# Kernel optimization log

Measured on AMD Instinct MI355X. Metric: run time of the kernel, lower is better.

The kernel has to match this reference:

```python
import jax, jax.numpy as jnp
import numpy as np

PARAM = 10.0
EPS = 1e-06

def _feature_map(t):
    # elus_feature_map: param*relu(x) + (exp(param*min(x,0)) - 1) + 1
    x1 = jax.nn.relu(t)
    x2 = t - x1  # negative part
    return PARAM * x1 + jnp.exp(PARAM * x2)

def setup_inputs() -> dict:
    key = jax.random.key(0)
    ks = jax.random.split(key, 7)
    B, C, H, W = 8, 512, 128, 128
    d = C // 8
    s = 1.0 / np.sqrt(C)
    return {
        "x":  jax.random.normal(ks[0], (B, C, H, W), dtype=jnp.float32),
        "Wq": jax.random.normal(ks[1], (d, C), dtype=jnp.float32) * s,
        "bq": jax.random.normal(ks[2], (d,), dtype=jnp.float32) * 0.01,
        "Wk": jax.random.normal(ks[3], (d, C), dtype=jnp.float32) * s,
        "bk": jax.random.normal(ks[4], (d,), dtype=jnp.float32) * 0.01,
        "Wv": jax.random.normal(ks[5], (C, C), dtype=jnp.float32) * s,
        "bv": jax.random.normal(ks[6], (C,), dtype=jnp.float32) * 0.01,
        "gamma": jnp.full((1,), 0.5, dtype=jnp.float32),
    }

def reference(x, Wq, bq, Wk, bk, Wv, bv, gamma):
    B, C, H, W = x.shape
    N = H * W
    xf = x.reshape(B, C, N)  # flatten spatial; 1x1 convs become matmuls
    Q = jnp.einsum('dc,bcn->bdn', Wq, xf) + bq[None, :, None]   # [B, d, N]
    K = jnp.einsum('dc,bcn->bdn', Wk, xf) + bk[None, :, None]   # [B, d, N]
    V = jnp.einsum('oc,bcn->bon', Wv, xf) + bv[None, :, None]   # [B, C, N]
    Q = jnp.transpose(_feature_map(Q), (0, 2, 1))               # [B, N, d]
    K = _feature_map(K)                                         # [B, d, N]
    KV = jnp.einsum('bmn,bcn->bmc', K, V)                       # [B, d, C]
    norm = 1.0 / jnp.einsum('bnc,bc->bn', Q, jnp.sum(K, axis=-1) + EPS)  # [B, N]
    wv = jnp.einsum('bnm,bmc,bn->bcn', Q, KV, norm)             # [B, C, N]
    wv = wv.reshape(B, C, H, W)
    return x + gamma * wv
```

## Files before the change

### kernel.cpp

```cpp
#include <hip/hip_runtime.h>
#include <hip/hip_bf16.h>
#include <cstdint>

typedef __bf16 bf16x8 __attribute__((ext_vector_type(8)));
typedef float f32x4 __attribute__((ext_vector_type(4)));

#define DEV static __device__ __forceinline__

constexpr int NB = 8;
constexpr int NC = 512;
constexpr int NS = 16384;
constexpr int ND = 64;
constexpr int SK = 32;
constexpr float FPARAM = 10.0f;
constexpr float FEPS = 1e-6f;

DEV unsigned short f2bf(float f) {
  uint32_t u = __builtin_bit_cast(uint32_t, f);
  u += 0x7fffu + ((u >> 16) & 1u);
  return (unsigned short)(u >> 16);
}
DEV float bf2f(unsigned short h) {
  uint32_t u = ((uint32_t)h) << 16;
  return __builtin_bit_cast(float, u);
}
DEV float fmap(float t) {
  float p = fmaxf(t, 0.0f);
  float m = fminf(t, 0.0f);
  return FPARAM * p + __expf(FPARAM * m);
}

DEV void tile_store4(unsigned short* t, int row, int k, ushort4 v) {
  int ch = (k >> 3) ^ (row & 7);
  *(ushort4*)(t + row * 64 + ch * 8 + (k & 7)) = v;
}
DEV void tile_store8(unsigned short* t, int row, int k, uint4 v) {
  int ch = (k >> 3) ^ (row & 7);
  *(uint4*)(t + row * 64 + ch * 8) = v;
}
DEV bf16x8 tile_frag(const unsigned short* t, int row, int k) {
  int ch = (k >> 3) ^ (row & 7);
  uint4 u = *(const uint4*)(t + row * 64 + ch * 8);
  return __builtin_bit_cast(bf16x8, u);
}
DEV f32x4 mfma16(bf16x8 a, bf16x8 b, f32x4 c) {
  return __builtin_amdgcn_mfma_f32_16x16x32_bf16(a, b, c, 0, 0, 0);
}

__global__ __launch_bounds__(256) void kernelA(
    const float* __restrict__ x, const float* __restrict__ Wq,
    const float* __restrict__ bq, const float* __restrict__ Wk,
    const float* __restrict__ bk, unsigned short* __restrict__ Kp,
    unsigned short* __restrict__ Qt) {
  __shared__ unsigned short sW[128 * 64];
  __shared__ unsigned short sX[128 * 64];
  const int t = threadIdx.x;
  const int lane = t & 63, wave = t >> 6;
  const int wm = wave >> 1, wn = wave & 1;
  const int l15 = lane & 15, q = lane >> 4;
  const int n0 = blockIdx.x * 128;
  const int b = blockIdx.y;
  const float* xb = x + (size_t)b * NC * NS;

  f32x4 acc[4][4];
  const f32x4 zero = {0.f, 0.f, 0.f, 0.f};
  for (int i = 0; i < 4; i++)
    for (int j = 0; j < 4; j++) acc[i][j] = zero;

  const int qq = t & 3, grp = t >> 2;
  const int n4 = (grp & 31) * 4, cb = (grp >> 5) * 4;
  const int shfl_base = (t & 63) & ~3;

  for (int c0 = 0; c0 < NC; c0 += 64) {
    __syncthreads();
    {
      int f4 = t & 15;
      for (int it = 0; it < 8; it++) {
        int row = (t >> 4) + it * 16;
        const float* src = (row < 64) ? (Wq + (size_t)row * NC + c0 + f4 * 4)
                                      : (Wk + (size_t)(row - 64) * NC + c0 + f4 * 4);
        float4 v = *(const float4*)src;
        tile_store4(sW, row, f4 * 4,
                    make_ushort4(f2bf(v.x), f2bf(v.y), f2bf(v.z), f2bf(v.w)));
      }
    }
    for (int it = 0; it < 8; it++) {
      int c_l = cb + qq + it * 8;
      float4 v = *(const float4*)(xb + (size_t)(c0 + c_l) * NS + n0 + n4);
      float vv[4] = {v.x, v.y, v.z, v.w};
      float o[4];
      for (int r = 0; r < 4; r++) {
        int j = (qq + r) & 3;
        float send = vv[(qq - r) & 3];
        o[j] = __shfl(send, shfl_base + j);
      }
      tile_store4(sX, n4 + qq, it * 8 + cb,
                  make_ushort4(f2bf(o[0]), f2bf(o[1]), f2bf(o[2]), f2bf(o[3])));
    }
    __syncthreads();
    for (int kk = 0; kk < 64; kk += 32) {
      int kb = kk + q * 8;
      bf16x8 af[4], bg[4];
      for (int i = 0; i < 4; i++) af[i] = tile_frag(sW, wm * 64 + i * 16 + l15, kb);
      for (int j = 0; j < 4; j++) bg[j] = tile_frag(sX, wn * 64 + j * 16 + l15, kb);
      for (int i = 0; i < 4; i++)
        for (int j = 0; j < 4; j++) acc[i][j] = mfma16(af[i], bg[j], acc[i][j]);
    }
  }

  if (wm == 0) {
    for (int i = 0; i < 4; i++) {
      int mb = i * 16 + q * 4;
      float b0 = bq[mb + 0], b1 = bq[mb + 1], b2 = bq[mb + 2], b3 = bq[mb + 3];
      for (int j = 0; j < 4; j++) {
        int n = n0 + wn * 64 + j * 16 + l15;
        f32x4 v = acc[i][j];
        ushort4 o = make_ushort4(f2bf(fmap(v[0] + b0)), f2bf(fmap(v[1] + b1)),
                                 f2bf(fmap(v[2] + b2)), f2bf(fmap(v[3] + b3)));
        *(ushort4*)(Qt + ((size_t)b * NS + n) * ND + mb) = o;
      }
    }
  } else {
    for (int i = 0; i < 4; i++) {
      int mb = i * 16 + q * 4;
      float b0 = bk[mb + 0], b1 = bk[mb + 1], b2 = bk[mb + 2], b3 = bk[mb + 3];
      for (int j = 0; j < 4; j++) {
        int n = n0 + wn * 64 + j * 16 + l15;
        f32x4 v = acc[i][j];
        Kp[((size_t)b * ND + mb + 0) * NS + n] = f2bf(fmap(v[0] + b0));
        Kp[((size_t)b * ND + mb + 1) * NS + n] = f2bf(fmap(v[1] + b1));
        Kp[((size_t)b * ND + mb + 2) * NS + n] = f2bf(fmap(v[2] + b2));
        Kp[((size_t)b * ND + mb + 3) * NS + n] = f2bf(fmap(v[3] + b3));
      }
    }
  }
}

__global__ __launch_bounds__(256) void kernelB(
    const float* __restrict__ x, const unsigned short* __restrict__ Kp,
    float* __restrict__ Pp, float* __restrict__ KsP) {
  __shared__ unsigned short sK[64 * 64];
  __shared__ unsigned short sX[256 * 64];
  __shared__ float sSum[64];
  const int t = threadIdx.x;
  const int lane = t & 63, wave = t >> 6;
  const int l15 = lane & 15, q = lane >> 4;
  const int s = blockIdx.x, half = blockIdx.y, b = blockIdx.z;
  const int cp0 = half * 256;
  const int nbase = s * (NS / SK);
  if (t < 64) sSum[t] = 0.0f;

  f32x4 acc[4][4];
  const f32x4 zero = {0.f, 0.f, 0.f, 0.f};
  for (int i = 0; i < 4; i++)
    for (int j = 0; j < 4; j++) acc[i][j] = zero;

  for (int nc = 0; nc < NS / SK; nc += 64) {
    int n0 = nbase + nc;
    __syncthreads();
    for (int it = 0; it < 2; it++) {
      int row = (t >> 3) + it * 32;
      int ch = t & 7;
      uint4 v = *(const uint4*)(Kp + ((size_t)b * ND + row) * NS + n0 + ch * 8);
      tile_store8(sK, row, ch * 8, v);
      if (half == 0) {
        const unsigned short* pv = (const unsigned short*)&v;
        float ssum = 0.f;
        for (int e = 0; e < 8; e++) ssum += bf2f(pv[e]);
        atomicAdd(&sSum[row], ssum);
      }
    }
    {
      int f4 = t & 15;
      for (int it = 0; it < 16; it++) {
        int row = (t >> 4) + it * 16;
        float4 v = *(const float4*)(x + ((size_t)b * NC + cp0 + row) * NS + n0 + f4 * 4);
        tile_store4(sX, row, f4 * 4,
                    make_ushort4(f2bf(v.x), f2bf(v.y), f2bf(v.z), f2bf(v.w)));
      }
    }
    __syncthreads();
    for (int kk = 0; kk < 64; kk += 32) {
      int kb = kk + q * 8;
      bf16x8 af[4], bg[4];
      for (int i = 0; i < 4; i++) af[i] = tile_frag(sK, i * 16 + l15, kb);
      for (int j = 0; j < 4; j++) bg[j] = tile_frag(sX, wave * 64 + j * 16 + l15, kb);
      for (int i = 0; i < 4; i++)
        for (int j = 0; j < 4; j++) acc[i][j] = mfma16(af[i], bg[j], acc[i][j]);
    }
  }
  for (int i = 0; i < 4; i++) {
    int mb = i * 16 + q * 4;
    for (int j = 0; j < 4; j++) {
      int cp = cp0 + wave * 64 + j * 16 + l15;
      f32x4 v = acc[i][j];
      for (int r = 0; r < 4; r++)
        Pp[(((size_t)b * SK + s) * ND + mb + r) * NC + cp] = v[r];
    }
  }
  __syncthreads();
  if (half == 0 && t < 64) KsP[((size_t)b * SK + s) * ND + t] = sSum[t];
}

__global__ __launch_bounds__(256) void kernelC1(
    const float* __restrict__ Pp, const float* __restrict__ KsP,
    float* __restrict__ KXt, float* __restrict__ Ksum) {
  const int m = blockIdx.x, b = blockIdx.y, t = threadIdx.x;
  float a0 = 0.f, a1 = 0.f;
  for (int s = 0; s < SK; s++) {
    const float* p = Pp + (((size_t)b * SK + s) * ND + m) * NC;
    a0 += p[t];
    a1 += p[t + 256];
  }
  float* o = KXt + ((size_t)b * ND + m) * NC;
  o[t] = a0;
  o[t + 256] = a1;
  if (t == 0) {
    float ks = 0.f;
    for (int s = 0; s < SK; s++) ks += KsP[((size_t)b * SK + s) * ND + m];
    Ksum[b * ND + m] = ks;
  }
}

__global__ __launch_bounds__(64) void kernelC2(
    const float* __restrict__ KXt, const float* __restrict__ Wv,
    const float* __restrict__ bv, const float* __restrict__ Ksum,
    unsigned short* __restrict__ KVT) {
  __shared__ unsigned short sA[64 * 64];
  __shared__ unsigned short sB[64 * 64];
  const int t = threadIdx.x;
  const int l15 = t & 15, q = t >> 4;
  const int ct = blockIdx.x, b = blockIdx.y;
  f32x4 acc[4][4];
  const f32x4 zero = {0.f, 0.f, 0.f, 0.f};
  for (int i = 0; i < 4; i++)
    for (int j = 0; j < 4; j++) acc[i][j] = zero;

  for (int c0 = 0; c0 < NC; c0 += 64) {
    __syncthreads();
    int f4 = t & 15;
    for (int it = 0; it < 16; it++) {
      int row = (t >> 4) + it * 4;
      float4 v = *(const float4*)(Wv + ((size_t)(ct * 64 + row)) * NC + c0 + f4 * 4);
      tile_store4(sA, row, f4 * 4,
                  make_ushort4(f2bf(v.x), f2bf(v.y), f2bf(v.z), f2bf(v.w)));
      float4 w = *(const float4*)(KXt + ((size_t)b * ND + row) * NC + c0 + f4 * 4);
      tile_store4(sB, row, f4 * 4,
                  make_ushort4(f2bf(w.x), f2bf(w.y), f2bf(w.z), f2bf(w.w)));
    }
    __syncthreads();
    for (int kk = 0; kk < 64; kk += 32) {
      int kb = kk + q * 8;
      bf16x8 af[4], bg[4];
      for (int i = 0; i < 4; i++) af[i] = tile_frag(sA, i * 16 + l15, kb);
      for (int j = 0; j < 4; j++) bg[j] = tile_frag(sB, j * 16 + l15, kb);
      for (int i = 0; i < 4; i++)
        for (int j = 0; j < 4; j++) acc[i][j] = mfma16(af[i], bg[j], acc[i][j]);
    }
  }
  for (int j = 0; j < 4; j++) {
    int m = j * 16 + l15;
    float ks = Ksum[b * ND + m];
    for (int i = 0; i < 4; i++) {
      for (int r = 0; r < 4; r++) {
        int c = ct * 64 + i * 16 + q * 4 + r;
        float v = acc[i][j][r] + ks * bv[c];
        KVT[((size_t)b * NC + c) * ND + m] = f2bf(v);
      }
    }
  }
}

__global__ __launch_bounds__(256) void kernelD(
    const float* __restrict__ x, const unsigned short* __restrict__ Qt,
    const unsigned short* __restrict__ KVT, const float* __restrict__ Ksum,
    const float* __restrict__ gamma, float* __restrict__ out) {
  __shared__ unsigned short sA[256 * 64];
  __shared__ unsigned short sB[128 * 64];
  __shared__ float sN[128];
  __shared__ float sKs[64];
  const int t = threadIdx.x;
  const int lane = t & 63, wave = t >> 6;
  const int wm = wave >> 1, wn = wave & 1;
  const int l15 = lane & 15, q = lane >> 4;
  const int n0 = blockIdx.x * 128;
  const int c0 = blockIdx.y * 256;
  const int b = blockIdx.z;
  if (t < 64) sKs[t] = Ksum[b * ND + t] + FEPS;
  {
    int ch = t & 7;
    for (int it = 0; it < 8; it++) {
      int row = (t >> 3) + it * 32;
      uint4 v = *(const uint4*)(KVT + ((size_t)b * NC + c0 + row) * ND + ch * 8);
      tile_store8(sA, row, ch * 8, v);
    }
    for (int it = 0; it < 4; it++) {
      int row = (t >> 3) + it * 32;
      uint4 v = *(const uint4*)(Qt + ((size_t)b * NS + n0 + row) * ND + ch * 8);
      tile_store8(sB, row, ch * 8, v);
    }
  }
  __syncthreads();
  if (t < 128) {
    float sum = 0.f;
    for (int ch = 0; ch < 8; ch++) {
      const unsigned short* p = sB + t * 64 + ((ch ^ (t & 7)) * 8);
      for (int e = 0; e < 8; e++) sum += bf2f(p[e]) * sKs[ch * 8 + e];
    }
    sN[t] = 1.0f / sum;
  }
  __syncthreads();

  f32x4 acc[8][4];
  const f32x4 zero = {0.f, 0.f, 0.f, 0.f};
  for (int i = 0; i < 8; i++)
    for (int j = 0; j < 4; j++) acc[i][j] = zero;
  for (int kk = 0; kk < 64; kk += 32) {
    int kb = kk + q * 8;
    bf16x8 af[8], bg[4];
    for (int i = 0; i < 8; i++) af[i] = tile_frag(sA, wm * 128 + i * 16 + l15, kb);
    for (int j = 0; j < 4; j++) bg[j] = tile_frag(sB, wn * 64 + j * 16 + l15, kb);
    for (int i = 0; i < 8; i++)
      for (int j = 0; j < 4; j++) acc[i][j] = mfma16(af[i], bg[j], acc[i][j]);
  }
  float g = gamma[0];
  for (int i = 0; i < 8; i++) {
    int cb = c0 + wm * 128 + i * 16 + q * 4;
    for (int j = 0; j < 4; j++) {
      int nl = wn * 64 + j * 16 + l15;
      int n = n0 + nl;
      float nr = sN[nl] * g;
      f32x4 v = acc[i][j];
      for (int r = 0; r < 4; r++) {
        size_t idx = ((size_t)b * NC + cb + r) * NS + n;
        out[idx] = x[idx] + nr * v[r];
      }
    }
  }
}

extern "C" void kernel_launch(void* const* d_in, const int* in_sizes, int n_in,
                              void* d_out, int out_size, void* d_ws, size_t ws_size,
                              hipStream_t stream) {
  (void)in_sizes; (void)n_in; (void)out_size; (void)ws_size;
  const float* x = (const float*)d_in[0];
  const float* Wq = (const float*)d_in[1];
  const float* bq = (const float*)d_in[2];
  const float* Wk = (const float*)d_in[3];
  const float* bk = (const float*)d_in[4];
  const float* Wv = (const float*)d_in[5];
  const float* bv = (const float*)d_in[6];
  const float* gamma = (const float*)d_in[7];
  float* out = (float*)d_out;

  char* ws = (char*)d_ws;
  unsigned short* Qt = (unsigned short*)ws;  ws += (size_t)NB * NS * ND * 2;
  unsigned short* Kp = (unsigned short*)ws;  ws += (size_t)NB * ND * NS * 2;
  float* Pp = (float*)ws;                    ws += (size_t)NB * SK * ND * NC * 4;
  float* KsP = (float*)ws;                   ws += (size_t)NB * SK * ND * 4;
  float* KXt = (float*)ws;                   ws += (size_t)NB * ND * NC * 4;
  float* Ksum = (float*)ws;                  ws += (size_t)NB * ND * 4;
  unsigned short* KVT = (unsigned short*)ws; ws += (size_t)NB * NC * ND * 2;

  kernelA<<<dim3(NS / 128, NB), dim3(256), 0, stream>>>(x, Wq, bq, Wk, bk, Kp, Qt);
  kernelB<<<dim3(SK, 2, NB), dim3(256), 0, stream>>>(x, Kp, Pp, KsP);
  kernelC1<<<dim3(ND, NB), dim3(256), 0, stream>>>(Pp, KsP, KXt, Ksum);
  kernelC2<<<dim3(NC / 64, NB), dim3(64), 0, stream>>>(KXt, Wv, bv, Ksum, KVT);
  kernelD<<<dim3(NS / 128, NC / 256, NB), dim3(256), 0, stream>>>(x, Qt, KVT, Ksum, gamma, out);
}
```

Before: 640.6 us.

## Pre-convert weights to bf16, drop LDS staging, fuse K-sum into projection kernel

Adds a prep kernel that converts Wq/Wk/Wv to bf16 once per call, so the projection and KV kernels read bf16 weight fragments straight from global memory. The K column-sum moves into kernelA's epilogue through wave shuffles and global atomics, which removes the partial-sum buffer and its reduction. kernelB, C2 and D drop shared-memory tiles and load MFMA fragments directly from global memory. kernelA double-buffers x in registers and LDS, and block indices are remapped for locality. The cost is an extra launch, float atomics whose summation order is nondeterministic, and uncoalesced direct global fragment loads.

After: 683.1 us. 6.6% more time.

```diff
diff --git a/kernel.cpp b/kernel.cpp
--- a/kernel.cpp
+++ b/kernel.cpp
@@ -1,9 +1,9 @@
 #include <hip/hip_runtime.h>
-#include <hip/hip_bf16.h>
 #include <cstdint>
 
 typedef __bf16 bf16x8 __attribute__((ext_vector_type(8)));
 typedef float f32x4 __attribute__((ext_vector_type(4)));
+typedef unsigned short u16x8 __attribute__((ext_vector_type(8)));
 
 #define DEV static __device__ __forceinline__
 
@@ -29,31 +29,58 @@
   float m = fminf(t, 0.0f);
   return FPARAM * p + __expf(FPARAM * m);
 }
+DEV f32x4 mfma16(bf16x8 a, bf16x8 b, f32x4 c) {
+  return __builtin_amdgcn_mfma_f32_16x16x32_bf16(a, b, c, 0, 0, 0);
+}
+DEV bf16x8 ld_bf8(const unsigned short* p) {
+  uint4 u = *(const uint4*)p;
+  return __builtin_bit_cast(bf16x8, u);
+}
+DEV bf16x8 cvt8(float4 a, float4 b) {
+  u16x8 t;
+  t[0] = f2bf(a.x); t[1] = f2bf(a.y); t[2] = f2bf(a.z); t[3] = f2bf(a.w);
+  t[4] = f2bf(b.x); t[5] = f2bf(b.y); t[6] = f2bf(b.z); t[7] = f2bf(b.w);
+  return __builtin_bit_cast(bf16x8, t);
+}
 
 DEV void tile_store4(unsigned short* t, int row, int k, ushort4 v) {
   int ch = (k >> 3) ^ (row & 7);
   *(ushort4*)(t + row * 64 + ch * 8 + (k & 7)) = v;
-}
-DEV void tile_store8(unsigned short* t, int row, int k, uint4 v) {
-  int ch = (k >> 3) ^ (row & 7);
-  *(uint4*)(t + row * 64 + ch * 8) = v;
 }
 DEV bf16x8 tile_frag(const unsigned short* t, int row, int k) {
   int ch = (k >> 3) ^ (row & 7);
   uint4 u = *(const uint4*)(t + row * 64 + ch * 8);
   return __builtin_bit_cast(bf16x8, u);
 }
-DEV f32x4 mfma16(bf16x8 a, bf16x8 b, f32x4 c) {
-  return __builtin_amdgcn_mfma_f32_16x16x32_bf16(a, b, c, 0, 0, 0);
+
+__global__ __launch_bounds__(256) void kernelP(
+    const float* __restrict__ Wq, const float* __restrict__ Wk,
+    const float* __restrict__ Wv, unsigned short* __restrict__ Wqkb,
+    unsigned short* __restrict__ Wvb, float* __restrict__ Ksum) {
+  const int tid = blockIdx.x * 256 + threadIdx.x;
+  const int stride = gridDim.x * 256;
+  if (tid < NB * ND) Ksum[tid] = 0.f;
+  for (int p = tid; p < ND * NC / 4; p += stride) {
+    float4 v = ((const float4*)Wq)[p];
+    ((ushort4*)Wqkb)[p] = make_ushort4(f2bf(v.x), f2bf(v.y), f2bf(v.z), f2bf(v.w));
+  }
+  for (int p = tid; p < ND * NC / 4; p += stride) {
+    float4 v = ((const float4*)Wk)[p];
+    ((ushort4*)(Wqkb + ND * NC))[p] =
+        make_ushort4(f2bf(v.x), f2bf(v.y), f2bf(v.z), f2bf(v.w));
+  }
+  for (int p = tid; p < NC * NC / 4; p += stride) {
+    float4 v = ((const float4*)Wv)[p];
+    ((ushort4*)Wvb)[p] = make_ushort4(f2bf(v.x), f2bf(v.y), f2bf(v.z), f2bf(v.w));
+  }
 }
 
 __global__ __launch_bounds__(256) void kernelA(
-    const float* __restrict__ x, const float* __restrict__ Wq,
-    const float* __restrict__ bq, const float* __restrict__ Wk,
-    const float* __restrict__ bk, unsigned short* __restrict__ Kp,
-    unsigned short* __restrict__ Qt) {
-  __shared__ unsigned short sW[128 * 64];
-  __shared__ unsigned short sX[128 * 64];
+    const float* __restrict__ x, const unsigned short* __restrict__ Wqk,
+    const float* __restrict__ bq, const float* __restrict__ bk,
+    unsigned short* __restrict__ Kp, unsigned short* __restrict__ Qt,
+    float* __restrict__ Ksum) {
+  __shared__ unsigned short sX[2][128 * 64];
   const int t = threadIdx.x;
   const int lane = t & 63, wave = t >> 6;
   const int wm = wave >> 1, wn = wave & 1;
@@ -69,49 +96,59 @@
 
   const int qq = t & 3, grp = t >> 2;
   const int n4 = (grp & 31) * 4, cb = (grp >> 5) * 4;
-  const int shfl_base = (t & 63) & ~3;
-
-  for (int c0 = 0; c0 < NC; c0 += 64) {
-    __syncthreads();
-    {
-      int f4 = t & 15;
-      for (int it = 0; it < 8; it++) {
-        int row = (t >> 4) + it * 16;
-        const float* src = (row < 64) ? (Wq + (size_t)row * NC + c0 + f4 * 4)
-                                      : (Wk + (size_t)(row - 64) * NC + c0 + f4 * 4);
-        float4 v = *(const float4*)src;
-        tile_store4(sW, row, f4 * 4,
-                    make_ushort4(f2bf(v.x), f2bf(v.y), f2bf(v.z), f2bf(v.w)));
-      }
-    }
+  const int shfl_base = lane & ~3;
+
+  float4 pf[8];
+#pragma unroll
+  for (int it = 0; it < 8; it++)
+    pf[it] = *(const float4*)(xb + (size_t)(cb + qq + it * 8) * NS + n0 + n4);
+
+  for (int cc = 0; cc < 8; cc++) {
+    unsigned short* sx = sX[cc & 1];
+    const int c0 = cc * 64;
+#pragma unroll
     for (int it = 0; it < 8; it++) {
-      int c_l = cb + qq + it * 8;
-      float4 v = *(const float4*)(xb + (size_t)(c0 + c_l) * NS + n0 + n4);
+      float4 v = pf[it];
       float vv[4] = {v.x, v.y, v.z, v.w};
       float o[4];
+#pragma unroll
       for (int r = 0; r < 4; r++) {
         int j = (qq + r) & 3;
         float send = vv[(qq - r) & 3];
         o[j] = __shfl(send, shfl_base + j);
       }
-      tile_store4(sX, n4 + qq, it * 8 + cb,
+      tile_store4(sx, n4 + qq, it * 8 + cb,
                   make_ushort4(f2bf(o[0]), f2bf(o[1]), f2bf(o[2]), f2bf(o[3])));
     }
+    if (cc < 7) {
+      const int c1 = c0 + 64;
+#pragma unroll
+      for (int it = 0; it < 8; it++)
+        pf[it] = *(const float4*)(xb + (size_t)(c1 + cb + qq + it * 8) * NS + n0 + n4);
+    }
     __syncthreads();
+#pragma unroll
     for (int kk = 0; kk < 64; kk += 32) {
       int kb = kk + q * 8;
       bf16x8 af[4], bg[4];
-      for (int i = 0; i < 4; i++) af[i] = tile_frag(sW, wm * 64 + i * 16 + l15, kb);
-      for (int j = 0; j < 4; j++) bg[j] = tile_frag(sX, wn * 64 + j * 16 + l15, kb);
+#pragma unroll
       for (int i = 0; i < 4; i++)
+        af[i] = ld_bf8(Wqk + (size_t)(wm * 64 + i * 16 + l15) * NC + c0 + kb);
+#pragma unroll
+      for (int j = 0; j < 4; j++) bg[j] = tile_frag(sx, wn * 64 + j * 16 + l15, kb);
+#pragma unroll
+      for (int i = 0; i < 4; i++)
+#pragma unroll
         for (int j = 0; j < 4; j++) acc[i][j] = mfma16(af[i], bg[j], acc[i][j]);
     }
   }
 
   if (wm == 0) {
+#pragma unroll
     for (int i = 0; i < 4; i++) {
       int mb = i * 16 + q * 4;
       float b0 = bq[mb + 0], b1 = bq[mb + 1], b2 = bq[mb + 2], b3 = bq[mb + 3];
+#pragma unroll
       for (int j = 0; j < 4; j++) {
         int n = n0 + wn * 64 + j * 16 + l15;
         f32x4 v = acc[i][j];
@@ -121,16 +158,35 @@
       }
     }
   } else {
+#pragma unroll
     for (int i = 0; i < 4; i++) {
       int mb = i * 16 + q * 4;
       float b0 = bk[mb + 0], b1 = bk[mb + 1], b2 = bk[mb + 2], b3 = bk[mb + 3];
+      float ks0 = 0.f, ks1 = 0.f, ks2 = 0.f, ks3 = 0.f;
+#pragma unroll
       for (int j = 0; j < 4; j++) {
         int n = n0 + wn * 64 + j * 16 + l15;
         f32x4 v = acc[i][j];
-        Kp[((size_t)b * ND + mb + 0) * NS + n] = f2bf(fmap(v[0] + b0));
-        Kp[((size_t)b * ND + mb + 1) * NS + n] = f2bf(fmap(v[1] + b1));
-        Kp[((size_t)b * ND + mb + 2) * NS + n] = f2bf(fmap(v[2] + b2));
-        Kp[((size_t)b * ND + mb + 3) * NS + n] = f2bf(fmap(v[3] + b3));
+        float f0 = fmap(v[0] + b0), f1 = fmap(v[1] + b1);
+        float f2 = fmap(v[2] + b2), f3 = fmap(v[3] + b3);
+        Kp[((size_t)b * ND + mb + 0) * NS + n] = f2bf(f0);
+        Kp[((size_t)b * ND + mb + 1) * NS + n] = f2bf(f1);
+        Kp[((size_t)b * ND + mb + 2) * NS + n] = f2bf(f2);
+        Kp[((size_t)b * ND + mb + 3) * NS + n] = f2bf(f3);
+        ks0 += f0; ks1 += f1; ks2 += f2; ks3 += f3;
+      }
+#pragma unroll
+      for (int ms = 1; ms < 16; ms <<= 1) {
+        ks0 += __shfl_xor(ks0, ms);
+        ks1 += __shfl_xor(ks1, ms);
+        ks2 += __shfl_xor(ks2, ms);
+        ks3 += __shfl_xor(ks3, ms);
+      }
+      if (l15 == 0) {
+        atomicAdd(&Ksum[b * ND + mb + 0], ks0);
+        atomicAdd(&Ksum[b * ND + mb + 1], ks1);
+        atomicAdd(&Ksum[b * ND + mb + 2], ks2);
+        atomicAdd(&Ksum[b * ND + mb + 3], ks3);
       }
     }
   }
@@ -138,75 +194,59 @@
 
 __global__ __launch_bounds__(256) void kernelB(
     const float* __restrict__ x, const unsigned short* __restrict__ Kp,
-    float* __restrict__ Pp, float* __restrict__ KsP) {
-  __shared__ unsigned short sK[64 * 64];
-  __shared__ unsigned short sX[256 * 64];
-  __shared__ float sSum[64];
+    float* __restrict__ Pp) {
   const int t = threadIdx.x;
   const int lane = t & 63, wave = t >> 6;
   const int l15 = lane & 15, q = lane >> 4;
-  const int s = blockIdx.x, half = blockIdx.y, b = blockIdx.z;
-  const int cp0 = half * 256;
+  const int id = blockIdx.x, b = blockIdx.y;
+  const int s = ((id >> 5) << 3) + (id & 7);
+  const int quarter = (id >> 3) & 3;
   const int nbase = s * (NS / SK);
-  if (t < 64) sSum[t] = 0.0f;
-
-  f32x4 acc[4][4];
+  const unsigned short* kpb = Kp + (size_t)b * ND * NS;
+  const float* xq = x + ((size_t)b * NC + quarter * 128 + wave * 32) * NS;
+
+  f32x4 acc[4][2];
   const f32x4 zero = {0.f, 0.f, 0.f, 0.f};
   for (int i = 0; i < 4; i++)
-    for (int j = 0; j < 4; j++) acc[i][j] = zero;
-
-  for (int nc = 0; nc < NS / SK; nc += 64) {
-    int n0 = nbase + nc;
-    __syncthreads();
-    for (int it = 0; it < 2; it++) {
-      int row = (t >> 3) + it * 32;
-      int ch = t & 7;
-      uint4 v = *(const uint4*)(Kp + ((size_t)b * ND + row) * NS + n0 + ch * 8);
-      tile_store8(sK, row, ch * 8, v);
-      if (half == 0) {
-        const unsigned short* pv = (const unsigned short*)&v;
-        float ssum = 0.f;
-        for (int e = 0; e < 8; e++) ssum += bf2f(pv[e]);
-        atomicAdd(&sSum[row], ssum);
-      }
-    }
-    {
-      int f4 = t & 15;
-      for (int it = 0; it < 16; it++) {
-        int row = (t >> 4) + it * 16;
-        float4 v = *(const float4*)(x + ((size_t)b * NC + cp0 + row) * NS + n0 + f4 * 4);
-        tile_store4(sX, row, f4 * 4,
-                    make_ushort4(f2bf(v.x), f2bf(v.y), f2bf(v.z), f2bf(v.w)));
-      }
-    }
-    __syncthreads();
-    for (int kk = 0; kk < 64; kk += 32) {
-      int kb = kk + q * 8;
-      bf16x8 af[4], bg[4];
-      for (int i = 0; i < 4; i++) af[i] = tile_frag(sK, i * 16 + l15, kb);
-      for (int j = 0; j < 4; j++) bg[j] = tile_frag(sX, wave * 64 + j * 16 + l15, kb);
-      for (int i = 0; i < 4; i++)
-        for (int j = 0; j < 4; j++) acc[i][j] = mfma16(af[i], bg[j], acc[i][j]);
-    }
-  }
+    for (int j = 0; j < 2; j++) acc[i][j] = zero;
+
+#pragma unroll 2
+  for (int nc = 0; nc < NS / SK; nc += 32) {
+    int nb = nbase + nc + q * 8;
+    bf16x8 af[4], bg[2];
+#pragma unroll
+    for (int i = 0; i < 4; i++)
+      af[i] = ld_bf8(kpb + (size_t)(i * 16 + l15) * NS + nb);
+#pragma unroll
+    for (int j = 0; j < 2; j++) {
+      const float* px = xq + (size_t)(j * 16 + l15) * NS + nb;
+      bg[j] = cvt8(*(const float4*)px, *(const float4*)(px + 4));
+    }
+#pragma unroll
+    for (int i = 0; i < 4; i++)
+#pragma unroll
+      for (int j = 0; j < 2; j++) acc[i][j] = mfma16(af[i], bg[j], acc[i][j]);
+  }
+
+  float* pp = Pp + ((size_t)b * SK + s) * ND * NC;
+#pragma unroll
   for (int i = 0; i < 4; i++) {
     int mb = i * 16 + q * 4;
-    for (int j = 0; j < 4; j++) {
-      int cp = cp0 + wave * 64 + j * 16 + l15;
+#pragma unroll
+    for (int j = 0; j < 2; j++) {
+      int cp = quarter * 128 + wave * 32 + j * 16 + l15;
       f32x4 v = acc[i][j];
-      for (int r = 0; r < 4; r++)
-        Pp[(((size_t)b * SK + s) * ND + mb + r) * NC + cp] = v[r];
-    }
-  }
-  __syncthreads();
-  if (half == 0 && t < 64) KsP[((size_t)b * SK + s) * ND + t] = sSum[t];
+#pragma unroll
+      for (int r = 0; r < 4; r++) pp[(size_t)(mb + r) * NC + cp] = v[r];
+    }
+  }
 }
 
 __global__ __launch_bounds__(256) void kernelC1(
-    const float* __restrict__ Pp, const float* __restrict__ KsP,
-    float* __restrict__ KXt, float* __restrict__ Ksum) {
+    const float* __restrict__ Pp, float* __restrict__ KXt) {
   const int m = blockIdx.x, b = blockIdx.y, t = threadIdx.x;
   float a0 = 0.f, a1 = 0.f;
+#pragma unroll 8
   for (int s = 0; s < SK; s++) {
     const float* p = Pp + (((size_t)b * SK + s) * ND + m) * NC;
     a0 += p[t];
@@ -215,57 +255,52 @@
   float* o = KXt + ((size_t)b * ND + m) * NC;
   o[t] = a0;
   o[t + 256] = a1;
-  if (t == 0) {
-    float ks = 0.f;
-    for (int s = 0; s < SK; s++) ks += KsP[((size_t)b * SK + s) * ND + m];
-    Ksum[b * ND + m] = ks;
-  }
-}
-
-__global__ __launch_bounds__(64) void kernelC2(
-    const float* __restrict__ KXt, const float* __restrict__ Wv,
+}
+
+__global__ __launch_bounds__(256) void kernelC2(
+    const float* __restrict__ KXt, const unsigned short* __restrict__ Wvb,
     const float* __restrict__ bv, const float* __restrict__ Ksum,
     unsigned short* __restrict__ KVT) {
-  __shared__ unsigned short sA[64 * 64];
-  __shared__ unsigned short sB[64 * 64];
   const int t = threadIdx.x;
-  const int l15 = t & 15, q = t >> 4;
+  const int lane = t & 63, wave = t >> 6;
+  const int wm = wave >> 1, wn = wave & 1;
+  const int l15 = lane & 15, q = lane >> 4;
   const int ct = blockIdx.x, b = blockIdx.y;
-  f32x4 acc[4][4];
+
+  f32x4 acc[2][2];
   const f32x4 zero = {0.f, 0.f, 0.f, 0.f};
-  for (int i = 0; i < 4; i++)
-    for (int j = 0; j < 4; j++) acc[i][j] = zero;
-
-  for (int c0 = 0; c0 < NC; c0 += 64) {
-    __syncthreads();
-    int f4 = t & 15;
-    for (int it = 0; it < 16; it++) {
-      int row = (t >> 4) + it * 4;
-      float4 v = *(const float4*)(Wv + ((size_t)(ct * 64 + row)) * NC + c0 + f4 * 4);
-      tile_store4(sA, row, f4 * 4,
-                  make_ushort4(f2bf(v.x), f2bf(v.y), f2bf(v.z), f2bf(v.w)));
-      float4 w = *(const float4*)(KXt + ((size_t)b * ND + row) * NC + c0 + f4 * 4);
-      tile_store4(sB, row, f4 * 4,
-                  make_ushort4(f2bf(w.x), f2bf(w.y), f2bf(w.z), f2bf(w.w)));
-    }
-    __syncthreads();
-    for (int kk = 0; kk < 64; kk += 32) {
-      int kb = kk + q * 8;
-      bf16x8 af[4], bg[4];
-      for (int i = 0; i < 4; i++) af[i] = tile_frag(sA, i * 16 + l15, kb);
-      for (int j = 0; j < 4; j++) bg[j] = tile_frag(sB, j * 16 + l15, kb);
-      for (int i = 0; i < 4; i++)
-        for (int j = 0; j < 4; j++) acc[i][j] = mfma16(af[i], bg[j], acc[i][j]);
-    }
-  }
-  for (int j = 0; j < 4; j++) {
-    int m = j * 16 + l15;
-    float ks = Ksum[b * ND + m];
-    for (int i = 0; i < 4; i++) {
+  for (int i = 0; i < 2; i++)
+    for (int j = 0; j < 2; j++) acc[i][j] = zero;
+
+#pragma unroll 2
+  for (int c0 = 0; c0 < NC; c0 += 32) {
+    int kb = c0 + q * 8;
+    bf16x8 af[2], bg[2];
+#pragma unroll
+    for (int i = 0; i < 2; i++)
+      af[i] = ld_bf8(Wvb + (size_t)(ct * 64 + wm * 32 + i * 16 + l15) * NC + kb);
+#pragma unroll
+    for (int j = 0; j < 2; j++) {
+      const float* px = KXt + ((size_t)b * ND + wn * 32 + j * 16 + l15) * NC + kb;
+      bg[j] = cvt8(*(const float4*)px, *(const float4*)(px + 4));
+    }
+#pragma unroll
+    for (int i = 0; i < 2; i++)
+#pragma unroll
+      for (int j = 0; j < 2; j++) acc[i][j] = mfma16(af[i], bg[j], acc[i][j]);
+  }
+
+#pragma unroll
+  for (int j = 0; j < 2; j++) {
+    int m = wn * 32 + j * 16 + l15;
+    float km = Ksum[b * ND + m];
+#pragma unroll
+    for (int i = 0; i < 2; i++) {
+      f32x4 v = acc[i][j];
+#pragma unroll
       for (int r = 0; r < 4; r++) {
-        int c = ct * 64 + i * 16 + q * 4 + r;
-        float v = acc[i][j][r] + ks * bv[c];
-        KVT[((size_t)b * NC + c) * ND + m] = f2bf(v);
+        int c = ct * 64 + wm * 32 + i * 16 + q * 4 + r;
+        KVT[((size_t)b * NC + c) * ND + m] = f2bf(v[r] + km * bv[c]);
       }
     }
   }
@@ -275,65 +310,70 @@
     const float* __restrict__ x, const unsigned short* __restrict__ Qt,
     const unsigned short* __restrict__ KVT, const float* __restrict__ Ksum,
     const float* __restrict__ gamma, float* __restrict__ out) {
-  __shared__ unsigned short sA[256 * 64];
-  __shared__ unsigned short sB[128 * 64];
   __shared__ float sN[128];
   __shared__ float sKs[64];
   const int t = threadIdx.x;
   const int lane = t & 63, wave = t >> 6;
   const int wm = wave >> 1, wn = wave & 1;
   const int l15 = lane & 15, q = lane >> 4;
-  const int n0 = blockIdx.x * 128;
-  const int c0 = blockIdx.y * 256;
-  const int b = blockIdx.z;
+  const int id = blockIdx.x, b = blockIdx.y;
+  const int nblk = ((id >> 4) << 3) + (id & 7);
+  const int chalf = (id >> 3) & 1;
+  const int n0 = nblk * 128, c0 = chalf * 256;
+
   if (t < 64) sKs[t] = Ksum[b * ND + t] + FEPS;
-  {
-    int ch = t & 7;
-    for (int it = 0; it < 8; it++) {
-      int row = (t >> 3) + it * 32;
-      uint4 v = *(const uint4*)(KVT + ((size_t)b * NC + c0 + row) * ND + ch * 8);
-      tile_store8(sA, row, ch * 8, v);
-    }
-    for (int it = 0; it < 4; it++) {
-      int row = (t >> 3) + it * 32;
-      uint4 v = *(const uint4*)(Qt + ((size_t)b * NS + n0 + row) * ND + ch * 8);
-      tile_store8(sB, row, ch * 8, v);
-    }
-  }
   __syncthreads();
   if (t < 128) {
+    const unsigned short* qrow = Qt + ((size_t)b * NS + n0 + t) * ND;
     float sum = 0.f;
-    for (int ch = 0; ch < 8; ch++) {
-      const unsigned short* p = sB + t * 64 + ((ch ^ (t & 7)) * 8);
-      for (int e = 0; e < 8; e++) sum += bf2f(p[e]) * sKs[ch * 8 + e];
+#pragma unroll
+    for (int mm = 0; mm < 64; mm += 8) {
+      uint4 u = *(const uint4*)(qrow + mm);
+      const unsigned short* us = (const unsigned short*)&u;
+#pragma unroll
+      for (int e = 0; e < 8; e++) sum += bf2f(us[e]) * sKs[mm + e];
     }
     sN[t] = 1.0f / sum;
   }
   __syncthreads();
 
-  f32x4 acc[8][4];
-  const f32x4 zero = {0.f, 0.f, 0.f, 0.f};
-  for (int i = 0; i < 8; i++)
-    for (int j = 0; j < 4; j++) acc[i][j] = zero;
-  for (int kk = 0; kk < 64; kk += 32) {
-    int kb = kk + q * 8;
-    bf16x8 af[8], bg[4];
-    for (int i = 0; i < 8; i++) af[i] = tile_frag(sA, wm * 128 + i * 16 + l15, kb);
-    for (int j = 0; j < 4; j++) bg[j] = tile_frag(sB, wn * 64 + j * 16 + l15, kb);
-    for (int i = 0; i < 8; i++)
-      for (int j = 0; j < 4; j++) acc[i][j] = mfma16(af[i], bg[j], acc[i][j]);
-  }
-  float g = gamma[0];
-  for (int i = 0; i < 8; i++) {
-    int cb = c0 + wm * 128 + i * 16 + q * 4;
-    for (int j = 0; j < 4; j++) {
-      int nl = wn * 64 + j * 16 + l15;
-      int n = n0 + nl;
-      float nr = sN[nl] * g;
-      f32x4 v = acc[i][j];
-      for (int r = 0; r < 4; r++) {
-        size_t idx = ((size_t)b * NC + cb + r) * NS + n;
-        out[idx] = x[idx] + nr * v[r];
+  const float g = gamma[0];
+#pragma unroll 1
+  for (int h = 0; h < 2; h++) {
+    f32x4 acc[4][4];
+    const f32x4 zero = {0.f, 0.f, 0.f, 0.f};
+    for (int i = 0; i < 4; i++)
+      for (int j = 0; j < 4; j++) acc[i][j] = zero;
+#pragma unroll
+    for (int kk = 0; kk < 64; kk += 32) {
+      int kb = kk + q * 8;
+      bf16x8 af[4], bg[4];
+#pragma unroll
+      for (int i = 0; i < 4; i++)
+        af[i] = ld_bf8(KVT +
+                       ((size_t)b * NC + c0 + wm * 128 + h * 64 + i * 16 + l15) * ND + kb);
+#pragma unroll
+      for (int j = 0; j < 4; j++)
+        bg[j] = ld_bf8(Qt + ((size_t)b * NS + n0 + wn * 64 + j * 16 + l15) * ND + kb);
+#pragma unroll
+      for (int i = 0; i < 4; i++)
+#pragma unroll
+        for (int j = 0; j < 4; j++) acc[i][j] = mfma16(af[i], bg[j], acc[i][j]);
+    }
+#pragma unroll
+    for (int i = 0; i < 4; i++) {
+      int cb = c0 + wm * 128 + h * 64 + i * 16 + q * 4;
+#pragma unroll
+      for (int j = 0; j < 4; j++) {
+        int nl = wn * 64 + j * 16 + l15;
+        float nr = sN[nl] * g;
+        size_t base = ((size_t)b * NC + cb) * NS + n0 + nl;
+        f32x4 v = acc[i][j];
+#pragma unroll
+        for (int r = 0; r < 4; r++) {
+          size_t idx = base + (size_t)r * NS;
+          out[idx] = x[idx] + nr * v[r];
+        }
       }
     }
   }
@@ -357,14 +397,16 @@
   unsigned short* Qt = (unsigned short*)ws;  ws += (size_t)NB * NS * ND * 2;
   unsigned short* Kp = (unsigned short*)ws;  ws += (size_t)NB * ND * NS * 2;
   float* Pp = (float*)ws;                    ws += (size_t)NB * SK * ND * NC * 4;
-  float* KsP = (float*)ws;                   ws += (size_t)NB * SK * ND * 4;
   float* KXt = (float*)ws;                   ws += (size_t)NB * ND * NC * 4;
   float* Ksum = (float*)ws;                  ws += (size_t)NB * ND * 4;
   unsigned short* KVT = (unsigned short*)ws; ws += (size_t)NB * NC * ND * 2;
-
-  kernelA<<<dim3(NS / 128, NB), dim3(256), 0, stream>>>(x, Wq, bq, Wk, bk, Kp, Qt);
-  kernelB<<<dim3(SK, 2, NB), dim3(256), 0, stream>>>(x, Kp, Pp, KsP);
-  kernelC1<<<dim3(ND, NB), dim3(256), 0, stream>>>(Pp, KsP, KXt, Ksum);
-  kernelC2<<<dim3(NC / 64, NB), dim3(64), 0, stream>>>(KXt, Wv, bv, Ksum, KVT);
-  kernelD<<<dim3(NS / 128, NC / 256, NB), dim3(256), 0, stream>>>(x, Qt, KVT, Ksum, gamma, out);
-}
+  unsigned short* Wqkb = (unsigned short*)ws; ws += (size_t)2 * ND * NC * 2;
+  unsigned short* Wvb = (unsigned short*)ws;  ws += (size_t)NC * NC * 2;
+
+  kernelP<<<dim3(64), dim3(256), 0, stream>>>(Wq, Wk, Wv, Wqkb, Wvb, Ksum);
+  kernelA<<<dim3(NS / 128, NB), dim3(256), 0, stream>>>(x, Wqkb, bq, bk, Kp, Qt, Ksum);
+  kernelB<<<dim3(128, NB), dim3(256), 0, stream>>>(x, Kp, Pp);
+  kernelC1<<<dim3(ND, NB), dim3(256), 0, stream>>>(Pp, KXt);
+  kernelC2<<<dim3(NC / 64, NB), dim3(256), 0, stream>>>(KXt, Wvb, bv, Ksum, KVT);
+  kernelD<<<dim3(256, NB), dim3(256), 0, stream>>>(x, Qt, KVT, Ksum, gamma, out);
+}
```
